# Kernel optimization log

Measured on AMD Instinct MI355X. Metric: run time of the kernel, lower is better.

The kernel has to match this reference:

```python
import jax, jax.numpy as jnp
import numpy as np

IN_DIM = 784
HIDDEN = 512
STYLE = 128
BATCH = 2048
NUM_LABELS = 10


def setup_inputs() -> dict:
    key = jax.random.key(0)
    k1, k2, k3, k4 = jax.random.split(key, 4)
    x = jax.random.uniform(k1, (BATCH, IN_DIM), dtype=jnp.float32)
    m = jax.random.randint(k2, (BATCH,), 0, NUM_LABELS)
    # Embedding tables, scaled as in the torch __init__ (N(0,1)/fan)
    fc1_table = jax.random.normal(k3, (NUM_LABELS, (IN_DIM + 1) * HIDDEN), dtype=jnp.float32) / ((IN_DIM + 1) * HIDDEN)
    fc2_table = jax.random.normal(k4, (NUM_LABELS, (HIDDEN + 1) * STYLE), dtype=jnp.float32) / ((HIDDEN + 1) * STYLE)
    return {"x": x, "m": m, "fc1_table": fc1_table, "fc2_table": fc2_table}


def reference(x, m, fc1_table, fc2_table):
    B = x.shape[0]
    x = x.reshape(B, -1)  # [B, 784]
    # Per-sample weight matrices gathered by label
    fc1 = fc1_table[m].reshape(B, IN_DIM + 1, HIDDEN)   # [B, 785, H]
    fc1_w, fc1_b = fc1[:, :IN_DIM, :], fc1[:, -1, :]
    h1 = jax.nn.relu(jnp.einsum('bkj,bk->bj', fc1_w, x) + fc1_b)  # [B, H]
    fc2 = fc2_table[m].reshape(B, HIDDEN + 1, STYLE)    # [B, H+1, S]
    fc2_w, fc2_b = fc2[:, :HIDDEN, :], fc2[:, -1, :]
    h2 = jnp.einsum('bkj,bk->bj', fc2_w, h1) + fc2_b    # [B, S]
    return jax.nn.sigmoid(h2)
```

## Files before the change

kernel.cpp:

```cpp
#include <hip/hip_runtime.h>
#include <hip/hip_bf16.h>
#include <math.h>

#define BATCH      2048
#define IN_DIM     784
#define HIDDEN     512
#define STYLE      128
#define NUM_LABELS 10
#define FC1_STRIDE ((IN_DIM + 1) * HIDDEN)
#define FC2_STRIDE ((HIDDEN + 1) * STYLE)
#define KP1        800

#define TB        64
#define MAX_TILES 48
#define BK        32

#define META_NTILES 31
#define META_TILES  32
#define META_PERM   176

#define XB_OFF   16384ULL
#define W1B_OFF  (XB_OFF  + 2048ULL*KP1*2)
#define W2B_OFF  (W1B_OFF + 10ULL*512*KP1*2)
#define H1B_OFF  (W2B_OFF + 10ULL*128*512*2)
#define BF16_NEED (H1B_OFF + 2048ULL*512*2)

#define H1P_BYTE_OFF 16384ULL
#define FP32_NEED (H1P_BYTE_OFF + 2048ULL*512*4)

typedef short short8  __attribute__((ext_vector_type(8)));
typedef float float4e __attribute__((ext_vector_type(4)));

__device__ __forceinline__ ushort f2b(float v) {
    __hip_bfloat16 h = __float2bfloat16(v);
    return *reinterpret_cast<ushort*>(&h);
}

__global__ void k_meta(const int* __restrict__ m, int* __restrict__ meta) {
    __shared__ int cnt[NUM_LABELS], curs[NUM_LABELS], offs[NUM_LABELS + 1];
    __shared__ int permS[BATCH];
    const int tid = threadIdx.x;
    if (tid < NUM_LABELS) { cnt[tid] = 0; curs[tid] = 0; }
    __syncthreads();
    for (int b = tid; b < BATCH; b += 256) atomicAdd(&cnt[m[b]], 1);
    __syncthreads();
    if (tid == 0) {
        int off = 0;
        for (int L = 0; L < NUM_LABELS; ++L) { offs[L] = off; off += cnt[L]; }
        offs[NUM_LABELS] = off;
    }
    __syncthreads();
    for (int b = tid; b < BATCH; b += 256) {
        int L = m[b];
        int r = atomicAdd(&curs[L], 1);
        permS[offs[L] + r] = b;
    }
    __syncthreads();
    for (int i = tid; i < BATCH; i += 256) meta[META_PERM + i] = permS[i];
    if (tid == 0) {
        int idx = 0;
        for (int L = 0; L < NUM_LABELS; ++L) {
            int c = cnt[L], off = offs[L];
            for (int t = 0; t < c; t += TB) {
                meta[META_TILES + idx * 3 + 0] = L;
                meta[META_TILES + idx * 3 + 1] = off + t;
                meta[META_TILES + idx * 3 + 2] = min(TB, c - t);
                ++idx;
            }
        }
        meta[META_NTILES] = idx;
    }
}

__global__ void k_cvt_x(const float* __restrict__ x, ushort* __restrict__ xb) {
    const int row = blockIdx.y;
    const int k = blockIdx.x * 256 + threadIdx.x;
    if (k < KP1)
        xb[(size_t)row * KP1 + k] = (k < IN_DIM) ? f2b(x[(size_t)row * IN_DIM + k]) : 0;
}

__global__ void k_cvtT(const float* __restrict__ src, ushort* __restrict__ dst,
                       int Kvalid, int Kpad, int N,
                       size_t srcLstride, size_t dstLstride) {
    __shared__ float tile[32][33];
    const int k0 = blockIdx.x * 32, n0 = blockIdx.y * 32, L = blockIdx.z;
    const int tx = threadIdx.x, ty = threadIdx.y;
    for (int r = ty; r < 32; r += 8) {
        int k = k0 + r;
        tile[r][tx] = (k < Kvalid) ? src[(size_t)L * srcLstride + (size_t)k * N + n0 + tx] : 0.f;
    }
    __syncthreads();
    for (int r = ty; r < 32; r += 8) {
        int n = n0 + r;
        dst[(size_t)L * dstLstride + (size_t)n * Kpad + k0 + tx] = f2b(tile[tx][r]);
    }
}

__launch_bounds__(256)
__global__ void k_fc1m(const ushort* __restrict__ xb, const ushort* __restrict__ w1b,
                       const float* __restrict__ fc1t, const int* __restrict__ meta,
                       ushort* __restrict__ h1b) {
    const int t = blockIdx.x;
    if (t >= meta[META_NTILES]) return;
    const int L      = meta[META_TILES + 3 * t + 0];
    const int pstart = meta[META_TILES + 3 * t + 1];
    const int nrows  = meta[META_TILES + 3 * t + 2];
    const int col0   = blockIdx.y * 64;
    const ushort* __restrict__ W = w1b + (size_t)L * 512 * KP1;

    __shared__ int rows[TB];
    __shared__ __align__(16) ushort As[64][40];
    __shared__ __align__(16) ushort Bs[64][40];

    const int tid = threadIdx.x;
    if (tid < TB) rows[tid] = (tid < nrows) ? meta[META_PERM + pstart + tid] : -1;
    __syncthreads();

    const int sr = tid >> 2, sc = tid & 3;
    const int lane = tid & 63, wv = tid >> 6;
    const int qd = lane >> 4, ln16 = lane & 15;

    const int arow = rows[sr];
    const uint4* __restrict__ agp = (arow >= 0) ? (const uint4*)(xb + (size_t)arow * KP1) : nullptr;
    const uint4* __restrict__ bgp = (const uint4*)(W + (size_t)(col0 + sr) * KP1);

    float4e acc[4] = {};

    for (int k0 = 0; k0 < KP1; k0 += BK) {
        uint4 av = make_uint4(0u, 0u, 0u, 0u);
        if (agp) av = agp[(k0 >> 3) + sc];
        *(uint4*)&As[sr][sc * 8] = av;
        *(uint4*)&Bs[sr][sc * 8] = bgp[(k0 >> 3) + sc];
        __syncthreads();
        short8 a = *(const short8*)&As[wv * 16 + ln16][qd * 8];
#pragma unroll
        for (int nt = 0; nt < 4; ++nt) {
            short8 b = *(const short8*)&Bs[nt * 16 + ln16][qd * 8];
            acc[nt] = __builtin_amdgcn_mfma_f32_16x16x32_bf16(a, b, acc[nt], 0, 0, 0);
        }
        __syncthreads();
    }

    const float* __restrict__ bias = fc1t + (size_t)L * FC1_STRIDE + (size_t)IN_DIM * HIDDEN + col0;
#pragma unroll
    for (int nt = 0; nt < 4; ++nt) {
        const int c = nt * 16 + ln16;
        const float bs = bias[c];
#pragma unroll
        for (int i = 0; i < 4; ++i) {
            const int r = wv * 16 + qd * 4 + i;
            if (r < nrows)
                h1b[(size_t)(pstart + r) * HIDDEN + col0 + c] = f2b(fmaxf(acc[nt][i] + bs, 0.f));
        }
    }
}

__launch_bounds__(256)
__global__ void k_fc2m(const ushort* __restrict__ h1b, const ushort* __restrict__ w2b,
                       const float* __restrict__ fc2t, const int* __restrict__ meta,
                       float* __restrict__ out) {
    const int t = blockIdx.x;
    if (t >= meta[META_NTILES]) return;
    const int L      = meta[META_TILES + 3 * t + 0];
    const int pstart = meta[META_TILES + 3 * t + 1];
    const int nrows  = meta[META_TILES + 3 * t + 2];
    const int col0   = blockIdx.y * 64;
    const ushort* __restrict__ W = w2b + (size_t)L * 128 * 512;

    __shared__ int rows[TB];
    __shared__ __align__(16) ushort As[64][40];
    __shared__ __align__(16) ushort Bs[64][40];

    const int tid = threadIdx.x;
    if (tid < TB) rows[tid] = (tid < nrows) ? meta[META_PERM + pstart + tid] : -1;
    __syncthreads();

    const int sr = tid >> 2, sc = tid & 3;
    const int lane = tid & 63, wv = tid >> 6;
    const int qd = lane >> 4, ln16 = lane & 15;

    const bool aval = (sr < nrows);
    const uint4* __restrict__ agp = (const uint4*)(h1b + (size_t)(pstart + (aval ? sr : 0)) * HIDDEN);
    const uint4* __restrict__ bgp = (const uint4*)(W + (size_t)(col0 + sr) * 512);

    float4e acc[4] = {};

    for (int k0 = 0; k0 < HIDDEN; k0 += BK) {
        uint4 av = make_uint4(0u, 0u, 0u, 0u);
        if (aval) av = agp[(k0 >> 3) + sc];
        *(uint4*)&As[sr][sc * 8] = av;
        *(uint4*)&Bs[sr][sc * 8] = bgp[(k0 >> 3) + sc];
        __syncthreads();
        short8 a = *(const short8*)&As[wv * 16 + ln16][qd * 8];
#pragma unroll
        for (int nt = 0; nt < 4; ++nt) {
            short8 b = *(const short8*)&Bs[nt * 16 + ln16][qd * 8];
            acc[nt] = __builtin_amdgcn_mfma_f32_16x16x32_bf16(a, b, acc[nt], 0, 0, 0);
        }
        __syncthreads();
    }

    const float* __restrict__ bias = fc2t + (size_t)L * FC2_STRIDE + (size_t)HIDDEN * STYLE + col0;
#pragma unroll
    for (int nt = 0; nt < 4; ++nt) {
        const int c = nt * 16 + ln16;
        const float bs = bias[c];
#pragma unroll
        for (int i = 0; i < 4; ++i) {
            const int r = wv * 16 + qd * 4 + i;
            if (r < nrows) {
                const int orow = rows[r];
                out[(size_t)orow * STYLE + col0 + c] = 1.f / (1.f + __expf(-(acc[nt][i] + bs)));
            }
        }
    }
}

#define KC 16
__global__ void k_setup(const int* __restrict__ m, int* __restrict__ meta) {
    __shared__ int cnt[NUM_LABELS];
    int tid = threadIdx.x;
    if (tid < NUM_LABELS) cnt[tid] = 0;
    __syncthreads();
    for (int b = tid; b < BATCH; b += blockDim.x) atomicAdd(&cnt[m[b]], 1);
    __syncthreads();
    if (tid == 0) {
        int off = 0, idx = 0;
        for (int L = 0; L < NUM_LABELS; ++L) {
            int c = cnt[L];
            meta[L] = c; meta[10 + L] = 0; meta[20 + L] = off;
            for (int t = 0; t < c; t += TB) {
                meta[META_TILES + idx * 3 + 0] = L;
                meta[META_TILES + idx * 3 + 1] = off + t;
                meta[META_TILES + idx * 3 + 2] = min(TB, c - t);
                ++idx;
            }
            off += c;
        }
        meta[30] = off; meta[META_NTILES] = idx;
        for (int t = idx; t < MAX_TILES; ++t) {
            meta[META_TILES + t * 3 + 0] = 0;
            meta[META_TILES + t * 3 + 1] = 0;
            meta[META_TILES + t * 3 + 2] = 0;
        }
    }
}
__global__ void k_scatter(const int* __restrict__ m, int* __restrict__ meta) {
    int b = blockIdx.x * blockDim.x + threadIdx.x;
    if (b >= BATCH) return;
    int L = m[b];
    int r = atomicAdd(&meta[10 + L], 1);
    meta[META_PERM + meta[20 + L] + r] = b;
}
__launch_bounds__(256)
__global__ void k_fc1(const float* __restrict__ x, const float* __restrict__ fc1t,
                      const int* __restrict__ meta, float* __restrict__ h1p) {
    int t = blockIdx.x;
    if (t >= meta[META_NTILES]) return;
    const int L = meta[META_TILES + 3 * t + 0], pstart = meta[META_TILES + 3 * t + 1],
              nrows = meta[META_TILES + 3 * t + 2], col0 = blockIdx.y * 64;
    const float* __restrict__ W = fc1t + (size_t)L * FC1_STRIDE;
    __shared__ int rows[TB];
    __shared__ float As[KC][TB + 4];
    __shared__ float Bs[KC][64];
    const int tid = threadIdx.x;
    if (tid < TB) rows[tid] = (tid < nrows) ? meta[META_PERM + pstart + tid] : -1;
    __syncthreads();
    const int tr = tid >> 4, tc = tid & 15;
    const int ai = tid >> 2, ak = (tid & 3) * 4;
    const int bk = tid >> 4, bj = (tid & 15) * 4;
    const int arow = rows[ai];
    const float* __restrict__ xrow = x + (size_t)(arow < 0 ? 0 : arow) * IN_DIM;
    const bool aval = (arow >= 0);
    float acc[4][4] = {};
    for (int k0 = 0; k0 < IN_DIM; k0 += KC) {
        float4 av = make_float4(0.f, 0.f, 0.f, 0.f);
        if (aval) av = *(const float4*)(xrow + k0 + ak);
        As[ak + 0][ai] = av.x; As[ak + 1][ai] = av.y; As[ak + 2][ai] = av.z; As[ak + 3][ai] = av.w;
        *(float4*)&Bs[bk][bj] = *(const float4*)(W + (size_t)(k0 + bk) * HIDDEN + col0 + bj);
        __syncthreads();
#pragma unroll
        for (int kk = 0; kk < KC; ++kk) {
            float4 a = *(const float4*)&As[kk][tr * 4];
            float4 b = *(const float4*)&Bs[kk][tc * 4];
#pragma unroll
            for (int i = 0; i < 4; ++i) {
                float av2 = (&a.x)[i];
                acc[i][0] = fmaf(av2, b.x, acc[i][0]); acc[i][1] = fmaf(av2, b.y, acc[i][1]);
                acc[i][2] = fmaf(av2, b.z, acc[i][2]); acc[i][3] = fmaf(av2, b.w, acc[i][3]);
            }
        }
        __syncthreads();
    }
    const float4 bias = *(const float4*)(W + (size_t)IN_DIM * HIDDEN + col0 + tc * 4);
#pragma unroll
    for (int i = 0; i < 4; ++i) {
        int r = tr * 4 + i;
        if (r < nrows) {
            float4 v;
            v.x = fmaxf(acc[i][0] + bias.x, 0.f); v.y = fmaxf(acc[i][1] + bias.y, 0.f);
            v.z = fmaxf(acc[i][2] + bias.z, 0.f); v.w = fmaxf(acc[i][3] + bias.w, 0.f);
            *(float4*)(h1p + (size_t)(pstart + r) * HIDDEN + col0 + tc * 4) = v;
        }
    }
}
__launch_bounds__(256)
__global__ void k_fc2(const float* __restrict__ h1p, const float* __restrict__ fc2t,
                      const int* __restrict__ meta, float* __restrict__ out) {
    int t = blockIdx.x;
    if (t >= meta[META_NTILES]) return;
    const int L = meta[META_TILES + 3 * t + 0], pstart = meta[META_TILES + 3 * t + 1],
              nrows = meta[META_TILES + 3 * t + 2], col0 = blockIdx.y * 64;
    const float* __restrict__ W = fc2t + (size_t)L * FC2_STRIDE;
    __shared__ int rows[TB];
    __shared__ float As[KC][TB + 4];
    __shared__ float Bs[KC][64];
    const int tid = threadIdx.x;
    if (tid < TB) rows[tid] = (tid < nrows) ? meta[META_PERM + pstart + tid] : -1;
    __syncthreads();
    const int tr = tid >> 4, tc = tid & 15;
    const int ai = tid >> 2, ak = (tid & 3) * 4;
    const int bk = tid >> 4, bj = (tid & 15) * 4;
    const bool aval = (ai < nrows);
    float acc[4][4] = {};
    for (int k0 = 0; k0 < HIDDEN; k0 += KC) {
        float4 av = make_float4(0.f, 0.f, 0.f, 0.f);
        if (aval) av = *(const float4*)(h1p + (size_t)(pstart + ai) * HIDDEN + k0 + ak);
        As[ak + 0][ai] = av.x; As[ak + 1][ai] = av.y; As[ak + 2][ai] = av.z; As[ak + 3][ai] = av.w;
        *(float4*)&Bs[bk][bj] = *(const float4*)(W + (size_t)(k0 + bk) * STYLE + col0 + bj);
        __syncthreads();
#pragma unroll
        for (int kk = 0; kk < KC; ++kk) {
            float4 a = *(const float4*)&As[kk][tr * 4];
            float4 b = *(const float4*)&Bs[kk][tc * 4];
#pragma unroll
            for (int i = 0; i < 4; ++i) {
                float av2 = (&a.x)[i];
                acc[i][0] = fmaf(av2, b.x, acc[i][0]); acc[i][1] = fmaf(av2, b.y, acc[i][1]);
                acc[i][2] = fmaf(av2, b.z, acc[i][2]); acc[i][3] = fmaf(av2, b.w, acc[i][3]);
            }
        }
        __syncthreads();
    }
    const float4 bias = *(const float4*)(W + (size_t)HIDDEN * STYLE + col0 + tc * 4);
#pragma unroll
    for (int i = 0; i < 4; ++i) {
        int r = tr * 4 + i;
        if (r < nrows) {
            int orow = rows[r];
            float4 v;
            v.x = 1.f / (1.f + __expf(-(acc[i][0] + bias.x)));
            v.y = 1.f / (1.f + __expf(-(acc[i][1] + bias.y)));
            v.z = 1.f / (1.f + __expf(-(acc[i][2] + bias.z)));
            v.w = 1.f / (1.f + __expf(-(acc[i][3] + bias.w)));
            *(float4*)(out + (size_t)orow * STYLE + col0 + tc * 4) = v;
        }
    }
}
__launch_bounds__(256)
__global__ void k_naive(const float* __restrict__ x, const int* __restrict__ m,
                        const float* __restrict__ fc1t, const float* __restrict__ fc2t,
                        float* __restrict__ out) {
    __shared__ float xs[IN_DIM];
    __shared__ float h1[HIDDEN];
    const int b = blockIdx.x, tid = threadIdx.x, L = m[b];
    for (int k = tid; k < IN_DIM; k += 256) xs[k] = x[(size_t)b * IN_DIM + k];
    __syncthreads();
    const float* __restrict__ W1 = fc1t + (size_t)L * FC1_STRIDE;
    for (int j = tid; j < HIDDEN; j += 256) {
        float acc = W1[(size_t)IN_DIM * HIDDEN + j];
        for (int k = 0; k < IN_DIM; ++k) acc = fmaf(xs[k], W1[(size_t)k * HIDDEN + j], acc);
        h1[j] = fmaxf(acc, 0.f);
    }
    __syncthreads();
    const float* __restrict__ W2 = fc2t + (size_t)L * FC2_STRIDE;
    for (int j = tid; j < STYLE; j += 256) {
        float acc = W2[(size_t)HIDDEN * STYLE + j];
        for (int k = 0; k < HIDDEN; ++k) acc = fmaf(h1[k], W2[(size_t)k * STYLE + j], acc);
        out[(size_t)b * STYLE + j] = 1.f / (1.f + __expf(-acc));
    }
}

extern "C" void kernel_launch(void* const* d_in, const int* in_sizes, int n_in,
                              void* d_out, int out_size, void* d_ws, size_t ws_size,
                              hipStream_t stream) {
    const float* x    = (const float*)d_in[0];
    const int*   m    = (const int*)d_in[1];
    const float* fc1t = (const float*)d_in[2];
    const float* fc2t = (const float*)d_in[3];
    float* out = (float*)d_out;

    if (ws_size >= BF16_NEED) {
        int*    meta = (int*)d_ws;
        ushort* xb   = (ushort*)((char*)d_ws + XB_OFF);
        ushort* w1b  = (ushort*)((char*)d_ws + W1B_OFF);
        ushort* w2b  = (ushort*)((char*)d_ws + W2B_OFF);
        ushort* h1b  = (ushort*)((char*)d_ws + H1B_OFF);

        k_meta<<<1, 256, 0, stream>>>(m, meta);
        k_cvt_x<<<dim3((KP1 + 255) / 256, BATCH), 256, 0, stream>>>(x, xb);
        k_cvtT<<<dim3(KP1 / 32, HIDDEN / 32, NUM_LABELS), dim3(32, 8), 0, stream>>>(
            fc1t, w1b, IN_DIM, KP1, HIDDEN, (size_t)FC1_STRIDE, (size_t)512 * KP1);
        k_cvtT<<<dim3(HIDDEN / 32, STYLE / 32, NUM_LABELS), dim3(32, 8), 0, stream>>>(
            fc2t, w2b, HIDDEN, HIDDEN, STYLE, (size_t)FC2_STRIDE, (size_t)128 * 512);
        k_fc1m<<<dim3(MAX_TILES, HIDDEN / 64), 256, 0, stream>>>(xb, w1b, fc1t, meta, h1b);
        k_fc2m<<<dim3(MAX_TILES, STYLE / 64), 256, 0, stream>>>(h1b, w2b, fc2t, meta, out);
    } else if (ws_size >= FP32_NEED) {
        int*   meta = (int*)d_ws;
        float* h1p  = (float*)((char*)d_ws + H1P_BYTE_OFF);
        k_setup<<<1, 256, 0, stream>>>(m, meta);
        k_scatter<<<(BATCH + 255) / 256, 256, 0, stream>>>(m, meta);
        k_fc1<<<dim3(MAX_TILES, HIDDEN / 64), 256, 0, stream>>>(x, fc1t, meta, h1p);
        k_fc2<<<dim3(MAX_TILES, STYLE / 64), 256, 0, stream>>>(h1p, fc2t, meta, out);
    } else {
        k_naive<<<BATCH, 256, 0, stream>>>(x, m, fc1t, fc2t, out);
    }
}
```

Baseline: 122.1 us.

## Merge prep kernels, convert x to bf16 inside fc1, and double the K tile

The metadata build and both weight transpose-convert passes now run as one prep kernel, which removes two launches. The separate x-to-bf16 conversion kernel is dropped: fc1 loads fp32 rows of x directly and converts them to bf16 while staging into shared memory. The K tile grows from 32 to 64 (KP1 padded to 832), so each shared-memory stage feeds two MFMA sub-steps and there are half as many barriers. The cost is more register pressure and conversion work inside the GEMM loop, plus reads of the uncompressed fp32 x. The fp32 fallback path is removed.

Measured after the change: 107.0 us. -12.4%, faster.

```diff
diff --git a/kernel.cpp b/kernel.cpp
--- a/kernel.cpp
+++ b/kernel.cpp
@@ -9,24 +9,27 @@
 #define NUM_LABELS 10
 #define FC1_STRIDE ((IN_DIM + 1) * HIDDEN)
 #define FC2_STRIDE ((HIDDEN + 1) * STYLE)
-#define KP1        800
+#define KP1        832
 
 #define TB        64
 #define MAX_TILES 48
-#define BK        32
+#define BK        64
 
 #define META_NTILES 31
 #define META_TILES  32
 #define META_PERM   176
 
-#define XB_OFF   16384ULL
-#define W1B_OFF  (XB_OFF  + 2048ULL*KP1*2)
-#define W2B_OFF  (W1B_OFF + 10ULL*512*KP1*2)
-#define H1B_OFF  (W2B_OFF + 10ULL*128*512*2)
-#define BF16_NEED (H1B_OFF + 2048ULL*512*2)
-
-#define H1P_BYTE_OFF 16384ULL
-#define FP32_NEED (H1P_BYTE_OFF + 2048ULL*512*4)
+#define W1B_OFF  16384ULL
+#define W2B_OFF  (W1B_OFF + 10ULL*HIDDEN*KP1*2)
+#define H1B_OFF  (W2B_OFF + 10ULL*STYLE*HIDDEN*2)
+#define BF16_NEED (H1B_OFF + (size_t)BATCH*HIDDEN*2)
+
+#define W1_KB 26
+#define W1_NB 16
+#define W2_KB 16
+#define W2_NB 4
+#define W1_BLOCKS (W1_KB*W1_NB*NUM_LABELS)
+#define W2_BLOCKS (W2_KB*W2_NB*NUM_LABELS)
 
 typedef short short8  __attribute__((ext_vector_type(8)));
 typedef float float4e __attribute__((ext_vector_type(4)));
@@ -36,68 +39,77 @@
     return *reinterpret_cast<ushort*>(&h);
 }
 
-__global__ void k_meta(const int* __restrict__ m, int* __restrict__ meta) {
+__global__ void k_prep(const int* __restrict__ m, const float* __restrict__ fc1t,
+                       const float* __restrict__ fc2t, int* __restrict__ meta,
+                       ushort* __restrict__ w1b, ushort* __restrict__ w2b) {
+    const int tid = threadIdx.x;
+    int bid = blockIdx.x;
+
     __shared__ int cnt[NUM_LABELS], curs[NUM_LABELS], offs[NUM_LABELS + 1];
     __shared__ int permS[BATCH];
-    const int tid = threadIdx.x;
-    if (tid < NUM_LABELS) { cnt[tid] = 0; curs[tid] = 0; }
-    __syncthreads();
-    for (int b = tid; b < BATCH; b += 256) atomicAdd(&cnt[m[b]], 1);
-    __syncthreads();
-    if (tid == 0) {
-        int off = 0;
-        for (int L = 0; L < NUM_LABELS; ++L) { offs[L] = off; off += cnt[L]; }
-        offs[NUM_LABELS] = off;
-    }
-    __syncthreads();
-    for (int b = tid; b < BATCH; b += 256) {
-        int L = m[b];
-        int r = atomicAdd(&curs[L], 1);
-        permS[offs[L] + r] = b;
-    }
-    __syncthreads();
-    for (int i = tid; i < BATCH; i += 256) meta[META_PERM + i] = permS[i];
-    if (tid == 0) {
-        int idx = 0;
-        for (int L = 0; L < NUM_LABELS; ++L) {
-            int c = cnt[L], off = offs[L];
-            for (int t = 0; t < c; t += TB) {
-                meta[META_TILES + idx * 3 + 0] = L;
-                meta[META_TILES + idx * 3 + 1] = off + t;
-                meta[META_TILES + idx * 3 + 2] = min(TB, c - t);
-                ++idx;
+    __shared__ float tile[32][33];
+
+    if (bid == 0) {
+        if (tid < NUM_LABELS) { cnt[tid] = 0; curs[tid] = 0; }
+        __syncthreads();
+        for (int b = tid; b < BATCH; b += 256) atomicAdd(&cnt[m[b]], 1);
+        __syncthreads();
+        if (tid == 0) {
+            int off = 0;
+            for (int L = 0; L < NUM_LABELS; ++L) { offs[L] = off; off += cnt[L]; }
+            offs[NUM_LABELS] = off;
+        }
+        __syncthreads();
+        for (int b = tid; b < BATCH; b += 256) {
+            int L = m[b];
+            int r = atomicAdd(&curs[L], 1);
+            permS[offs[L] + r] = b;
+        }
+        __syncthreads();
+        for (int i = tid; i < BATCH; i += 256) meta[META_PERM + i] = permS[i];
+        if (tid == 0) {
+            int idx = 0;
+            for (int L = 0; L < NUM_LABELS; ++L) {
+                int c = cnt[L], off = offs[L];
+                for (int t = 0; t < c; t += TB) {
+                    meta[META_TILES + idx * 3 + 0] = L;
+                    meta[META_TILES + idx * 3 + 1] = off + t;
+                    meta[META_TILES + idx * 3 + 2] = min(TB, c - t);
+                    ++idx;
+                }
             }
-        }
-        meta[META_NTILES] = idx;
-    }
-}
-
-__global__ void k_cvt_x(const float* __restrict__ x, ushort* __restrict__ xb) {
-    const int row = blockIdx.y;
-    const int k = blockIdx.x * 256 + threadIdx.x;
-    if (k < KP1)
-        xb[(size_t)row * KP1 + k] = (k < IN_DIM) ? f2b(x[(size_t)row * IN_DIM + k]) : 0;
-}
-
-__global__ void k_cvtT(const float* __restrict__ src, ushort* __restrict__ dst,
-                       int Kvalid, int Kpad, int N,
-                       size_t srcLstride, size_t dstLstride) {
-    __shared__ float tile[32][33];
-    const int k0 = blockIdx.x * 32, n0 = blockIdx.y * 32, L = blockIdx.z;
-    const int tx = threadIdx.x, ty = threadIdx.y;
+            meta[META_NTILES] = idx;
+        }
+        return;
+    }
+
+    bid -= 1;
+    const float* src; ushort* dst; int Kvalid, Kpad, N, kb, nb, L; size_t srcL, dstL;
+    if (bid < W1_BLOCKS) {
+        kb = bid % W1_KB; nb = (bid / W1_KB) % W1_NB; L = bid / (W1_KB * W1_NB);
+        src = fc1t; dst = w1b; Kvalid = IN_DIM; Kpad = KP1; N = HIDDEN;
+        srcL = FC1_STRIDE; dstL = (size_t)HIDDEN * KP1;
+    } else {
+        bid -= W1_BLOCKS;
+        kb = bid % W2_KB; nb = (bid / W2_KB) % W2_NB; L = bid / (W2_KB * W2_NB);
+        src = fc2t; dst = w2b; Kvalid = HIDDEN; Kpad = HIDDEN; N = STYLE;
+        srcL = FC2_STRIDE; dstL = (size_t)STYLE * HIDDEN;
+    }
+    const int tx = tid & 31, ty = tid >> 5;
+    const int k0 = kb * 32, n0 = nb * 32;
     for (int r = ty; r < 32; r += 8) {
         int k = k0 + r;
-        tile[r][tx] = (k < Kvalid) ? src[(size_t)L * srcLstride + (size_t)k * N + n0 + tx] : 0.f;
+        tile[r][tx] = (k < Kvalid) ? src[(size_t)L * srcL + (size_t)k * N + n0 + tx] : 0.f;
     }
     __syncthreads();
     for (int r = ty; r < 32; r += 8) {
         int n = n0 + r;
-        dst[(size_t)L * dstLstride + (size_t)n * Kpad + k0 + tx] = f2b(tile[tx][r]);
+        dst[(size_t)L * dstL + (size_t)n * Kpad + k0 + tx] = f2b(tile[tx][r]);
     }
 }
 
 __launch_bounds__(256)
-__global__ void k_fc1m(const ushort* __restrict__ xb, const ushort* __restrict__ w1b,
+__global__ void k_fc1m(const float* __restrict__ x, const ushort* __restrict__ w1b,
                        const float* __restrict__ fc1t, const int* __restrict__ meta,
                        ushort* __restrict__ h1b) {
     const int t = blockIdx.x;
@@ -106,11 +118,11 @@
     const int pstart = meta[META_TILES + 3 * t + 1];
     const int nrows  = meta[META_TILES + 3 * t + 2];
     const int col0   = blockIdx.y * 64;
-    const ushort* __restrict__ W = w1b + (size_t)L * 512 * KP1;
+    const ushort* __restrict__ W = w1b + (size_t)L * HIDDEN * KP1 + (size_t)col0 * KP1;
 
     __shared__ int rows[TB];
-    __shared__ __align__(16) ushort As[64][40];
-    __shared__ __align__(16) ushort Bs[64][40];
+    __shared__ __align__(16) ushort As[64][72];
+    __shared__ __align__(16) ushort Bs[64][72];
 
     const int tid = threadIdx.x;
     if (tid < TB) rows[tid] = (tid < nrows) ? meta[META_PERM + pstart + tid] : -1;
@@ -121,22 +133,41 @@
     const int qd = lane >> 4, ln16 = lane & 15;
 
     const int arow = rows[sr];
-    const uint4* __restrict__ agp = (arow >= 0) ? (const uint4*)(xb + (size_t)arow * KP1) : nullptr;
-    const uint4* __restrict__ bgp = (const uint4*)(W + (size_t)(col0 + sr) * KP1);
+    const float* __restrict__ xr = x + (size_t)(arow < 0 ? 0 : arow) * IN_DIM;
+    const uint4* __restrict__ bgp = (const uint4*)(W + (size_t)sr * KP1);
 
     float4e acc[4] = {};
 
     for (int k0 = 0; k0 < KP1; k0 += BK) {
-        uint4 av = make_uint4(0u, 0u, 0u, 0u);
-        if (agp) av = agp[(k0 >> 3) + sc];
-        *(uint4*)&As[sr][sc * 8] = av;
-        *(uint4*)&Bs[sr][sc * 8] = bgp[(k0 >> 3) + sc];
-        __syncthreads();
-        short8 a = *(const short8*)&As[wv * 16 + ln16][qd * 8];
-#pragma unroll
-        for (int nt = 0; nt < 4; ++nt) {
-            short8 b = *(const short8*)&Bs[nt * 16 + ln16][qd * 8];
-            acc[nt] = __builtin_amdgcn_mfma_f32_16x16x32_bf16(a, b, acc[nt], 0, 0, 0);
+        const int ka = k0 + sc * 16;
+        float4 a0 = make_float4(0.f, 0.f, 0.f, 0.f), a1 = a0, a2 = a0, a3 = a0;
+        if (arow >= 0) {
+            if (ka      < IN_DIM) a0 = *(const float4*)(xr + ka);
+            if (ka + 4  < IN_DIM) a1 = *(const float4*)(xr + ka + 4);
+            if (ka + 8  < IN_DIM) a2 = *(const float4*)(xr + ka + 8);
+            if (ka + 12 < IN_DIM) a3 = *(const float4*)(xr + ka + 12);
+        }
+        uint4 b0 = bgp[(k0 >> 3) + sc * 2 + 0];
+        uint4 b1 = bgp[(k0 >> 3) + sc * 2 + 1];
+
+        ushort av[16];
+        av[0]=f2b(a0.x); av[1]=f2b(a0.y); av[2]=f2b(a0.z); av[3]=f2b(a0.w);
+        av[4]=f2b(a1.x); av[5]=f2b(a1.y); av[6]=f2b(a1.z); av[7]=f2b(a1.w);
+        av[8]=f2b(a2.x); av[9]=f2b(a2.y); av[10]=f2b(a2.z); av[11]=f2b(a2.w);
+        av[12]=f2b(a3.x); av[13]=f2b(a3.y); av[14]=f2b(a3.z); av[15]=f2b(a3.w);
+        *(uint4*)&As[sr][sc * 16 + 0] = *(const uint4*)&av[0];
+        *(uint4*)&As[sr][sc * 16 + 8] = *(const uint4*)&av[8];
+        *(uint4*)&Bs[sr][sc * 16 + 0] = b0;
+        *(uint4*)&Bs[sr][sc * 16 + 8] = b1;
+        __syncthreads();
+#pragma unroll
+        for (int s = 0; s < 2; ++s) {
+            short8 a = *(const short8*)&As[wv * 16 + ln16][s * 32 + qd * 8];
+#pragma unroll
+            for (int nt = 0; nt < 4; ++nt) {
+                short8 b = *(const short8*)&Bs[nt * 16 + ln16][s * 32 + qd * 8];
+                acc[nt] = __builtin_amdgcn_mfma_f32_16x16x32_bf16(a, b, acc[nt], 0, 0, 0);
+            }
         }
         __syncthreads();
     }
@@ -165,11 +196,11 @@
     const int pstart = meta[META_TILES + 3 * t + 1];
     const int nrows  = meta[META_TILES + 3 * t + 2];
     const int col0   = blockIdx.y * 64;
-    const ushort* __restrict__ W = w2b + (size_t)L * 128 * 512;
+    const ushort* __restrict__ W = w2b + (size_t)L * STYLE * HIDDEN + (size_t)col0 * HIDDEN;
 
     __shared__ int rows[TB];
-    __shared__ __align__(16) ushort As[64][40];
-    __shared__ __align__(16) ushort Bs[64][40];
+    __shared__ __align__(16) ushort As[64][72];
+    __shared__ __align__(16) ushort Bs[64][72];
 
     const int tid = threadIdx.x;
     if (tid < TB) rows[tid] = (tid < nrows) ? meta[META_PERM + pstart + tid] : -1;
@@ -181,21 +212,31 @@
 
     const bool aval = (sr < nrows);
     const uint4* __restrict__ agp = (const uint4*)(h1b + (size_t)(pstart + (aval ? sr : 0)) * HIDDEN);
-    const uint4* __restrict__ bgp = (const uint4*)(W + (size_t)(col0 + sr) * 512);
+    const uint4* __restrict__ bgp = (const uint4*)(W + (size_t)sr * HIDDEN);
 
     float4e acc[4] = {};
 
     for (int k0 = 0; k0 < HIDDEN; k0 += BK) {
-        uint4 av = make_uint4(0u, 0u, 0u, 0u);
-        if (aval) av = agp[(k0 >> 3) + sc];
-        *(uint4*)&As[sr][sc * 8] = av;
-        *(uint4*)&Bs[sr][sc * 8] = bgp[(k0 >> 3) + sc];
-        __syncthreads();
-        short8 a = *(const short8*)&As[wv * 16 + ln16][qd * 8];
-#pragma unroll
-        for (int nt = 0; nt < 4; ++nt) {
-            short8 b = *(const short8*)&Bs[nt * 16 + ln16][qd * 8];
-            acc[nt] = __builtin_amdgcn_mfma_f32_16x16x32_bf16(a, b, acc[nt], 0, 0, 0);
+        uint4 a0 = make_uint4(0u, 0u, 0u, 0u), a1 = a0;
+        if (aval) {
+            a0 = agp[(k0 >> 3) + sc * 2 + 0];
+            a1 = agp[(k0 >> 3) + sc * 2 + 1];
+        }
+        uint4 b0 = bgp[(k0 >> 3) + sc * 2 + 0];
+        uint4 b1 = bgp[(k0 >> 3) + sc * 2 + 1];
+        *(uint4*)&As[sr][sc * 16 + 0] = a0;
+        *(uint4*)&As[sr][sc * 16 + 8] = a1;
+        *(uint4*)&Bs[sr][sc * 16 + 0] = b0;
+        *(uint4*)&Bs[sr][sc * 16 + 8] = b1;
+        __syncthreads();
+#pragma unroll
+        for (int s = 0; s < 2; ++s) {
+            short8 a = *(const short8*)&As[wv * 16 + ln16][s * 32 + qd * 8];
+#pragma unroll
+            for (int nt = 0; nt < 4; ++nt) {
+                short8 b = *(const short8*)&Bs[nt * 16 + ln16][s * 32 + qd * 8];
+                acc[nt] = __builtin_amdgcn_mfma_f32_16x16x32_bf16(a, b, acc[nt], 0, 0, 0);
+            }
         }
         __syncthreads();
     }
@@ -216,147 +257,6 @@
     }
 }
 
-#define KC 16
-__global__ void k_setup(const int* __restrict__ m, int* __restrict__ meta) {
-    __shared__ int cnt[NUM_LABELS];
-    int tid = threadIdx.x;
-    if (tid < NUM_LABELS) cnt[tid] = 0;
-    __syncthreads();
-    for (int b = tid; b < BATCH; b += blockDim.x) atomicAdd(&cnt[m[b]], 1);
-    __syncthreads();
-    if (tid == 0) {
-        int off = 0, idx = 0;
-        for (int L = 0; L < NUM_LABELS; ++L) {
-            int c = cnt[L];
-            meta[L] = c; meta[10 + L] = 0; meta[20 + L] = off;
-            for (int t = 0; t < c; t += TB) {
-                meta[META_TILES + idx * 3 + 0] = L;
-                meta[META_TILES + idx * 3 + 1] = off + t;
-                meta[META_TILES + idx * 3 + 2] = min(TB, c - t);
-                ++idx;
-            }
-            off += c;
-        }
-        meta[30] = off; meta[META_NTILES] = idx;
-        for (int t = idx; t < MAX_TILES; ++t) {
-            meta[META_TILES + t * 3 + 0] = 0;
-            meta[META_TILES + t * 3 + 1] = 0;
-            meta[META_TILES + t * 3 + 2] = 0;
-        }
-    }
-}
-__global__ void k_scatter(const int* __restrict__ m, int* __restrict__ meta) {
-    int b = blockIdx.x * blockDim.x + threadIdx.x;
-    if (b >= BATCH) return;
-    int L = m[b];
-    int r = atomicAdd(&meta[10 + L], 1);
-    meta[META_PERM + meta[20 + L] + r] = b;
-}
-__launch_bounds__(256)
-__global__ void k_fc1(const float* __restrict__ x, const float* __restrict__ fc1t,
-                      const int* __restrict__ meta, float* __restrict__ h1p) {
-    int t = blockIdx.x;
-    if (t >= meta[META_NTILES]) return;
-    const int L = meta[META_TILES + 3 * t + 0], pstart = meta[META_TILES + 3 * t + 1],
-              nrows = meta[META_TILES + 3 * t + 2], col0 = blockIdx.y * 64;
-    const float* __restrict__ W = fc1t + (size_t)L * FC1_STRIDE;
-    __shared__ int rows[TB];
-    __shared__ float As[KC][TB + 4];
-    __shared__ float Bs[KC][64];
-    const int tid = threadIdx.x;
-    if (tid < TB) rows[tid] = (tid < nrows) ? meta[META_PERM + pstart + tid] : -1;
-    __syncthreads();
-    const int tr = tid >> 4, tc = tid & 15;
-    const int ai = tid >> 2, ak = (tid & 3) * 4;
-    const int bk = tid >> 4, bj = (tid & 15) * 4;
-    const int arow = rows[ai];
-    const float* __restrict__ xrow = x + (size_t)(arow < 0 ? 0 : arow) * IN_DIM;
-    const bool aval = (arow >= 0);
-    float acc[4][4] = {};
-    for (int k0 = 0; k0 < IN_DIM; k0 += KC) {
-        float4 av = make_float4(0.f, 0.f, 0.f, 0.f);
-        if (aval) av = *(const float4*)(xrow + k0 + ak);
-        As[ak + 0][ai] = av.x; As[ak + 1][ai] = av.y; As[ak + 2][ai] = av.z; As[ak + 3][ai] = av.w;
-        *(float4*)&Bs[bk][bj] = *(const float4*)(W + (size_t)(k0 + bk) * HIDDEN + col0 + bj);
-        __syncthreads();
-#pragma unroll
-        for (int kk = 0; kk < KC; ++kk) {
-            float4 a = *(const float4*)&As[kk][tr * 4];
-            float4 b = *(const float4*)&Bs[kk][tc * 4];
-#pragma unroll
-            for (int i = 0; i < 4; ++i) {
-                float av2 = (&a.x)[i];
-                acc[i][0] = fmaf(av2, b.x, acc[i][0]); acc[i][1] = fmaf(av2, b.y, acc[i][1]);
-                acc[i][2] = fmaf(av2, b.z, acc[i][2]); acc[i][3] = fmaf(av2, b.w, acc[i][3]);
-            }
-        }
-        __syncthreads();
-    }
-    const float4 bias = *(const float4*)(W + (size_t)IN_DIM * HIDDEN + col0 + tc * 4);
-#pragma unroll
-    for (int i = 0; i < 4; ++i) {
-        int r = tr * 4 + i;
-        if (r < nrows) {
-            float4 v;
-            v.x = fmaxf(acc[i][0] + bias.x, 0.f); v.y = fmaxf(acc[i][1] + bias.y, 0.f);
-            v.z = fmaxf(acc[i][2] + bias.z, 0.f); v.w = fmaxf(acc[i][3] + bias.w, 0.f);
-            *(float4*)(h1p + (size_t)(pstart + r) * HIDDEN + col0 + tc * 4) = v;
-        }
-    }
-}
-__launch_bounds__(256)
-__global__ void k_fc2(const float* __restrict__ h1p, const float* __restrict__ fc2t,
-                      const int* __restrict__ meta, float* __restrict__ out) {
-    int t = blockIdx.x;
-    if (t >= meta[META_NTILES]) return;
-    const int L = meta[META_TILES + 3 * t + 0], pstart = meta[META_TILES + 3 * t + 1],
-              nrows = meta[META_TILES + 3 * t + 2], col0 = blockIdx.y * 64;
-    const float* __restrict__ W = fc2t + (size_t)L * FC2_STRIDE;
-    __shared__ int rows[TB];
-    __shared__ float As[KC][TB + 4];
-    __shared__ float Bs[KC][64];
-    const int tid = threadIdx.x;
-    if (tid < TB) rows[tid] = (tid < nrows) ? meta[META_PERM + pstart + tid] : -1;
-    __syncthreads();
-    const int tr = tid >> 4, tc = tid & 15;
-    const int ai = tid >> 2, ak = (tid & 3) * 4;
-    const int bk = tid >> 4, bj = (tid & 15) * 4;
-    const bool aval = (ai < nrows);
-    float acc[4][4] = {};
-    for (int k0 = 0; k0 < HIDDEN; k0 += KC) {
-        float4 av = make_float4(0.f, 0.f, 0.f, 0.f);
-        if (aval) av = *(const float4*)(h1p + (size_t)(pstart + ai) * HIDDEN + k0 + ak);
-        As[ak + 0][ai] = av.x; As[ak + 1][ai] = av.y; As[ak + 2][ai] = av.z; As[ak + 3][ai] = av.w;
-        *(float4*)&Bs[bk][bj] = *(const float4*)(W + (size_t)(k0 + bk) * STYLE + col0 + bj);
-        __syncthreads();
-#pragma unroll
-        for (int kk = 0; kk < KC; ++kk) {
-            float4 a = *(const float4*)&As[kk][tr * 4];
-            float4 b = *(const float4*)&Bs[kk][tc * 4];
-#pragma unroll
-            for (int i = 0; i < 4; ++i) {
-                float av2 = (&a.x)[i];
-                acc[i][0] = fmaf(av2, b.x, acc[i][0]); acc[i][1] = fmaf(av2, b.y, acc[i][1]);
-                acc[i][2] = fmaf(av2, b.z, acc[i][2]); acc[i][3] = fmaf(av2, b.w, acc[i][3]);
-            }
-        }
-        __syncthreads();
-    }
-    const float4 bias = *(const float4*)(W + (size_t)HIDDEN * STYLE + col0 + tc * 4);
-#pragma unroll
-    for (int i = 0; i < 4; ++i) {
-        int r = tr * 4 + i;
-        if (r < nrows) {
-            int orow = rows[r];
-            float4 v;
-            v.x = 1.f / (1.f + __expf(-(acc[i][0] + bias.x)));
-            v.y = 1.f / (1.f + __expf(-(acc[i][1] + bias.y)));
-            v.z = 1.f / (1.f + __expf(-(acc[i][2] + bias.z)));
-            v.w = 1.f / (1.f + __expf(-(acc[i][3] + bias.w)));
-            *(float4*)(out + (size_t)orow * STYLE + col0 + tc * 4) = v;
-        }
-    }
-}
 __launch_bounds__(256)
 __global__ void k_naive(const float* __restrict__ x, const int* __restrict__ m,
                         const float* __restrict__ fc1t, const float* __restrict__ fc2t,
@@ -392,26 +292,13 @@
 
     if (ws_size >= BF16_NEED) {
         int*    meta = (int*)d_ws;
-        ushort* xb   = (ushort*)((char*)d_ws + XB_OFF);
         ushort* w1b  = (ushort*)((char*)d_ws + W1B_OFF);
         ushort* w2b  = (ushort*)((char*)d_ws + W2B_OFF);
         ushort* h1b  = (ushort*)((char*)d_ws + H1B_OFF);
 
-        k_meta<<<1, 256, 0, stream>>>(m, meta);
-        k_cvt_x<<<dim3((KP1 + 255) / 256, BATCH), 256, 0, stream>>>(x, xb);
-        k_cvtT<<<dim3(KP1 / 32, HIDDEN / 32, NUM_LABELS), dim3(32, 8), 0, stream>>>(
-            fc1t, w1b, IN_DIM, KP1, HIDDEN, (size_t)FC1_STRIDE, (size_t)512 * KP1);
-        k_cvtT<<<dim3(HIDDEN / 32, STYLE / 32, NUM_LABELS), dim3(32, 8), 0, stream>>>(
-            fc2t, w2b, HIDDEN, HIDDEN, STYLE, (size_t)FC2_STRIDE, (size_t)128 * 512);
-        k_fc1m<<<dim3(MAX_TILES, HIDDEN / 64), 256, 0, stream>>>(xb, w1b, fc1t, meta, h1b);
+        k_prep<<<1 + W1_BLOCKS + W2_BLOCKS, 256, 0, stream>>>(m, fc1t, fc2t, meta, w1b, w2b);
+        k_fc1m<<<dim3(MAX_TILES, HIDDEN / 64), 256, 0, stream>>>(x, w1b, fc1t, meta, h1b);
         k_fc2m<<<dim3(MAX_TILES, STYLE / 64), 256, 0, stream>>>(h1b, w2b, fc2t, meta, out);
-    } else if (ws_size >= FP32_NEED) {
-        int*   meta = (int*)d_ws;
-        float* h1p  = (float*)((char*)d_ws + H1P_BYTE_OFF);
-        k_setup<<<1, 256, 0, stream>>>(m, meta);
-        k_scatter<<<(BATCH + 255) / 256, 256, 0, stream>>>(m, meta);
-        k_fc1<<<dim3(MAX_TILES, HIDDEN / 64), 256, 0, stream>>>(x, fc1t, meta, h1p);
-        k_fc2<<<dim3(MAX_TILES, STYLE / 64), 256, 0, stream>>>(h1p, fc2t, meta, out);
     } else {
         k_naive<<<BATCH, 256, 0, stream>>>(x, m, fc1t, fc2t, out);
     }
```
